# Optimization experiments

Hardware: AMD Instinct MI355X
Metric: run time of the kernel (lower is better)

The kernel has to match this reference:

```python
import jax, jax.numpy as jnp
import numpy as np

N, E, H, IN_FEAT, NUM_GRAPHS, NUM_CLASSES, L, HID = 50000, 600000, 128, 7, 256, 2, 5, 256
EPS_MSG = 1e-7
EPS_SOFTMAX = 1e-16
LN_EPS = 1e-5


def layer_norm(x, g, b):
    mu = jnp.mean(x, axis=-1, keepdims=True)
    var = jnp.mean((x - mu) ** 2, axis=-1, keepdims=True)
    return (x - mu) * jax.lax.rsqrt(var + LN_EPS) * g + b


def setup_inputs() -> dict:
    key = jax.random.key(0)
    ks = jax.random.split(key, 16)
    s = 0.05
    return {
        "x": jax.random.normal(ks[0], (N, IN_FEAT), jnp.float32),
        "edge_index": jax.random.randint(ks[1], (2, E), 0, N),
        "batch": jnp.sort(jax.random.randint(ks[2], (N,), 0, NUM_GRAPHS)),
        "enc_W": jax.random.normal(ks[3], (IN_FEAT, H), jnp.float32) * s,
        "enc_b": jnp.zeros((H,), jnp.float32),
        "t": jnp.ones((L,), jnp.float32),  # learn_t, init t=1.0
        "W1": jax.random.normal(ks[4], (L, H, HID), jnp.float32) * s,
        "b1": jnp.zeros((L, HID), jnp.float32),
        "g1": jnp.ones((L, HID), jnp.float32),
        "bb1": jnp.zeros((L, HID), jnp.float32),
        "W2": jax.random.normal(ks[5], (L, HID, H), jnp.float32) * s,
        "b2": jnp.zeros((L, H), jnp.float32),
        "ln_g": jnp.ones((L, H), jnp.float32),
        "ln_b": jnp.zeros((L, H), jnp.float32),
        "cls_W": jax.random.normal(ks[6], (H, NUM_CLASSES), jnp.float32) * s,
        "cls_b": jnp.zeros((NUM_CLASSES,), jnp.float32),
    }


def reference(x, edge_index, batch, enc_W, enc_b, t, W1, b1, g1, bb1, W2, b2, ln_g, ln_b, cls_W, cls_b):
    n = x.shape[0]
    src, dst = edge_index[0], edge_index[1]  # messages flow src -> dst
    h = x @ enc_W + enc_b  # node_encoder, [N, H]
    for i in range(t.shape[0]):  # DeepGCNLayer, block='res+'
        z = jax.nn.relu(layer_norm(h, ln_g[i], ln_b[i]))
        # GENConv message: relu(x_j) + eps (edge_attr is None)
        msg = jax.nn.relu(z[src]) + EPS_MSG  # [E, H]
        # scatter-softmax aggregation with temperature t
        logits = msg * t[i]
        m = jax.ops.segment_max(logits, dst, num_segments=n)  # [N, H]
        ex = jnp.exp(logits - m[dst])
        den = jax.ops.segment_sum(ex, dst, num_segments=n) + EPS_SOFTMAX
        agg = jax.ops.segment_sum(ex * msg, dst, num_segments=n) / den
        # GENConv update MLP: Linear -> LayerNorm -> ReLU -> Linear on (agg + x)
        out = agg + z
        hm = jax.nn.relu(layer_norm(out @ W1[i] + b1[i], g1[i], bb1[i]))
        h = h + (hm @ W2[i] + b2[i])  # residual
    pooled = jax.ops.segment_sum(h, batch, num_segments=NUM_GRAPHS)  # global_add_pool
    return pooled @ cls_W + cls_b
```

## Files before the change

kernel.cpp:

```cpp
#include <hip/hip_runtime.h>
#include <hip/hip_bf16.h>

#define HD 128
#define HIDD 256
#define EPS_MSG 1e-7f
#define EPS_SM 1e-16f
#define LN_EPS 1e-5f
#define HP2 264
#define LOG2E 1.44269504f

typedef __attribute__((ext_vector_type(8))) short bf16x8;
typedef __attribute__((ext_vector_type(4))) float f32x4;
typedef __attribute__((ext_vector_type(4))) ushort u16x4;

static __device__ __forceinline__ float wave_reduce_sum(float v) {
#pragma unroll
    for (int off = 32; off >= 1; off >>= 1) v += __shfl_xor(v, off, 64);
    return v;
}

static __device__ __forceinline__ float u2f(unsigned v) {
    union { float f; unsigned u; } x;
    x.u = v;
    return x.f;
}
static __device__ __forceinline__ ushort f2bf(float f) {
    __hip_bfloat16 b = __float2bfloat16(f);
    return *(ushort*)&b;
}
static __device__ __forceinline__ unsigned packbf(float lo, float hi) {
    return (unsigned)f2bf(lo) | ((unsigned)f2bf(hi) << 16);
}

__global__ __launch_bounds__(256) void enc_ln_kernel(const float* __restrict__ x,
                                                     const float* __restrict__ W,
                                                     const float* __restrict__ b,
                                                     const float* __restrict__ g,
                                                     const float* __restrict__ bt,
                                                     unsigned* __restrict__ hp,
                                                     unsigned* __restrict__ zp, int N) {
    int node = blockIdx.x * 4 + (threadIdx.x >> 6);
    int lane = threadIdx.x & 63;
    if (node >= N) return;
    float xr[7];
#pragma unroll
    for (int j = 0; j < 7; ++j) xr[j] = x[node * 7 + j];
    float v0 = b[lane], v1 = b[lane + 64];
#pragma unroll
    for (int j = 0; j < 7; ++j) {
        v0 = fmaf(xr[j], W[j * HD + lane], v0);
        v1 = fmaf(xr[j], W[j * HD + lane + 64], v1);
    }
    float s = wave_reduce_sum(v0 + v1);
    float ss = wave_reduce_sum(v0 * v0 + v1 * v1);
    float mu = s * (1.f / 128.f);
    float var = ss * (1.f / 128.f) - mu * mu;
    float rstd = rsqrtf(var + LN_EPS);
    float z0 = fmaxf((v0 - mu) * rstd * g[lane] + bt[lane], 0.f);
    float z1 = fmaxf((v1 - mu) * rstd * g[lane + 64] + bt[lane + 64], 0.f);
    int i0 = (2 * lane) & 63, i1 = (2 * lane + 1) & 63;
    float he_lo = __shfl(v0, i0), ho_lo = __shfl(v0, i1);
    float he_hi = __shfl(v1, i0), ho_hi = __shfl(v1, i1);
    float hce = (lane < 32) ? he_lo : he_hi;
    float hco = (lane < 32) ? ho_lo : ho_hi;
    hp[(size_t)node * 64 + lane] = packbf(hce, hco);
    float e_lo = __shfl(z0, i0), o_lo = __shfl(z0, i1);
    float e_hi = __shfl(z1, i0), o_hi = __shfl(z1, i1);
    float ce = (lane < 32) ? e_lo : e_hi;
    float co = (lane < 32) ? o_lo : o_hi;
    zp[(size_t)node * 64 + lane] = packbf(ce, co);
}

__global__ __launch_bounds__(256) void wconv_kernel(const float* __restrict__ W1,
                                                    const float* __restrict__ W2,
                                                    ushort* __restrict__ W1t,
                                                    ushort* __restrict__ W2t, int L) {
    int gid = blockIdx.x * 256 + threadIdx.x;
    int per = HD * HIDD;
    int tot = L * per;
    if (gid < tot) {
        int l = gid / per, r = gid % per;
        int n = r >> 7, k = r & 127;
        W1t[gid] = f2bf(W1[(size_t)l * per + (size_t)k * HIDD + n]);
    } else if (gid < 2 * tot) {
        int g2 = gid - tot;
        int l = g2 / per, r = g2 % per;
        int n = r >> 8, k = r & 255;
        W2t[g2] = f2bf(W2[(size_t)l * per + (size_t)k * HD + n]);
    }
}

__global__ __launch_bounds__(256) void count_kernel(const int* __restrict__ dst, int* __restrict__ cnt, int E) {
    int e = blockIdx.x * 256 + threadIdx.x;
    if (e < E) atomicAdd(&cnt[dst[e]], 1);
}

__global__ __launch_bounds__(256) void scanA_kernel(const int* __restrict__ cnt, int* __restrict__ row_ptr,
                                                    int* __restrict__ blk_sums, int n) {
    __shared__ int sb[256];
    int tid = threadIdx.x;
    int idx = blockIdx.x * 256 + tid;
    int v = (idx < n) ? cnt[idx] : 0;
    sb[tid] = v;
    __syncthreads();
#pragma unroll
    for (int off = 1; off < 256; off <<= 1) {
        int x = (tid >= off) ? sb[tid - off] : 0;
        __syncthreads();
        sb[tid] += x;
        __syncthreads();
    }
    if (idx < n) row_ptr[idx + 1] = sb[tid];
    if (tid == 255) blk_sums[blockIdx.x] = sb[255];
}

__global__ __launch_bounds__(256) void scanB_kernel(int* __restrict__ blk_sums, int nblk) {
    __shared__ int sb[256];
    int tid = threadIdx.x;
    int v = (tid < nblk) ? blk_sums[tid] : 0;
    sb[tid] = v;
    __syncthreads();
#pragma unroll
    for (int off = 1; off < 256; off <<= 1) {
        int x = (tid >= off) ? sb[tid - off] : 0;
        __syncthreads();
        sb[tid] += x;
        __syncthreads();
    }
    if (tid < nblk) blk_sums[tid] = sb[tid];
}

__global__ __launch_bounds__(256) void scanC_kernel(int* __restrict__ row_ptr, const int* __restrict__ blk_sums,
                                                    int* __restrict__ cursor, int n) {
    int idx = blockIdx.x * 256 + threadIdx.x;
    if (idx == 0) { row_ptr[0] = 0; cursor[0] = 0; }
    if (idx < n) {
        int b = idx >> 8;
        int v = row_ptr[idx + 1] + ((b > 0) ? blk_sums[b - 1] : 0);
        row_ptr[idx + 1] = v;
        if (idx + 1 < n) cursor[idx + 1] = v;
    }
}

__global__ __launch_bounds__(256) void scatter_kernel(const int* __restrict__ src, const int* __restrict__ dst,
                                                      int* __restrict__ cursor, int* __restrict__ esrc, int E) {
    int e = blockIdx.x * 256 + threadIdx.x;
    if (e < E) {
        int v = dst[e];
        int pos = atomicAdd(&cursor[v], 1);
        esrc[pos] = src[e];
    }
}

__global__ __launch_bounds__(256) void agg_kernel(const unsigned* __restrict__ zp,
                                                  const int* __restrict__ row_ptr,
                                                  const int* __restrict__ esrc,
                                                  const float* __restrict__ t_all, int layer,
                                                  unsigned* __restrict__ obuf, int N) {
    int node = __builtin_amdgcn_readfirstlane(blockIdx.x * 4 + (threadIdx.x >> 6));
    int lane = threadIdx.x & 63;
    if (node >= N) return;
    const float tv = t_all[layer];
    const float M = 12.f * fmaxf(tv, 1.f);
    const float tv2 = tv * LOG2E;
    const float mM2 = -M * LOG2E;
    int beg = row_ptr[node], end = row_ptr[node + 1];

    unsigned ps = zp[(size_t)node * 64 + lane];

    float se0 = 0.f, se1 = 0.f, sw0 = 0.f, sw1 = 0.f;
    float te0 = 0.f, te1 = 0.f, tw0 = 0.f, tw1 = 0.f;

#define AGG_EDGE(P, E0, E1, W0, W1)                                   \
    {                                                                  \
        float a0 = u2f((P) << 16) + EPS_MSG;                           \
        float a1 = u2f((P) & 0xffff0000u) + EPS_MSG;                   \
        float x0 = __builtin_amdgcn_exp2f(fmaf(a0, tv2, mM2));         \
        float x1 = __builtin_amdgcn_exp2f(fmaf(a1, tv2, mM2));         \
        E0 += x0;                                                      \
        E1 += x1;                                                      \
        W0 = fmaf(x0, a0, W0);                                         \
        W1 = fmaf(x1, a1, W1);                                         \
    }

    int e = beg;
    unsigned pc0, pc1, pc2, pc3;
    int have = 0;
    if (e + 4 <= end) {
        int s0 = esrc[e], s1 = esrc[e + 1], s2 = esrc[e + 2], s3 = esrc[e + 3];
        pc0 = zp[(size_t)s0 * 64 + lane];
        pc1 = zp[(size_t)s1 * 64 + lane];
        pc2 = zp[(size_t)s2 * 64 + lane];
        pc3 = zp[(size_t)s3 * 64 + lane];
        have = 4;
        e += 4;
    }
    while (have == 4) {
        unsigned pn0, pn1, pn2, pn3;
        int haven = 0;
        if (e + 4 <= end) {
            int s0 = esrc[e], s1 = esrc[e + 1], s2 = esrc[e + 2], s3 = esrc[e + 3];
            pn0 = zp[(size_t)s0 * 64 + lane];
            pn1 = zp[(size_t)s1 * 64 + lane];
            pn2 = zp[(size_t)s2 * 64 + lane];
            pn3 = zp[(size_t)s3 * 64 + lane];
            haven = 4;
            e += 4;
        }
        AGG_EDGE(pc0, se0, se1, sw0, sw1)
        AGG_EDGE(pc1, se0, se1, sw0, sw1)
        AGG_EDGE(pc2, te0, te1, tw0, tw1)
        AGG_EDGE(pc3, te0, te1, tw0, tw1)
        pc0 = pn0; pc1 = pn1; pc2 = pn2; pc3 = pn3;
        have = haven;
    }
    for (; e < end; ++e) {
        unsigned p0 = zp[(size_t)esrc[e] * 64 + lane];
        AGG_EDGE(p0, se0, se1, sw0, sw1)
    }
#undef AGG_EDGE
    se0 += te0; se1 += te1; sw0 += tw0; sw1 += tw1;

    float a0 = (end > beg) ? sw0 / (se0 + EPS_SM) : 0.f;
    float a1 = (end > beg) ? sw1 / (se1 + EPS_SM) : 0.f;
    float z0 = u2f(ps << 16), z1 = u2f(ps & 0xffff0000u);
    obuf[(size_t)node * 64 + lane] = packbf(a0 + z0, a1 + z1);
}

__global__ __launch_bounds__(256) void mlp_kernel(const ushort* __restrict__ obuf,
                                                  unsigned* __restrict__ hp,
                                                  const ushort* __restrict__ W1t, const float* __restrict__ b1,
                                                  const float* __restrict__ g1, const float* __restrict__ bb1,
                                                  const ushort* __restrict__ W2t, const float* __restrict__ b2,
                                                  const float* __restrict__ gnext, const float* __restrict__ btnext,
                                                  unsigned* __restrict__ zp, int fuse,
                                                  int ntiles, int N) {
    __shared__ ushort s_hm[32 * HP2];
    __shared__ float s_part[32 * 8];

    int tid = threadIdx.x;
    int wid = tid >> 6, lane = tid & 63;
    int l15 = lane & 15, q = lane >> 4;

    bf16x8 w1f[4][4];
#pragma unroll
    for (int kk = 0; kk < 4; ++kk)
#pragma unroll
        for (int nb = 0; nb < 4; ++nb)
            w1f[kk][nb] = *(const bf16x8*)&W1t[(size_t)(wid * 64 + nb * 16 + l15) * HD + kk * 32 + q * 8];
    bf16x8 w2f[8][2];
#pragma unroll
    for (int kk = 0; kk < 8; ++kk)
#pragma unroll
        for (int nb = 0; nb < 2; ++nb)
            w2f[kk][nb] = *(const bf16x8*)&W2t[(size_t)(wid * 32 + nb * 16 + l15) * HIDD + kk * 32 + q * 8];

    for (int tile = blockIdx.x; tile < ntiles; tile += gridDim.x) {
        int row0 = tile * 32;

        uint2 hpre[2][2];
        bf16x8 bfr[4][2];
#pragma unroll
        for (int mb = 0; mb < 2; ++mb) {
            int row = row0 + mb * 16 + l15;
            if (row < N) {
#pragma unroll
                for (int nb = 0; nb < 2; ++nb)
                    hpre[mb][nb] = *(const uint2*)&hp[(size_t)row * 64 + wid * 16 + nb * 8 + q * 2];
#pragma unroll
                for (int kk = 0; kk < 4; ++kk)
                    bfr[kk][mb] = *(const bf16x8*)(obuf + (size_t)row * HD + kk * 32 + q * 8);
            } else {
#pragma unroll
                for (int nb = 0; nb < 2; ++nb) { hpre[mb][nb].x = 0u; hpre[mb][nb].y = 0u; }
#pragma unroll
                for (int kk = 0; kk < 4; ++kk) bfr[kk][mb] = (bf16x8)0;
            }
        }
        __syncthreads();

        f32x4 acc1[2][4];
#pragma unroll
        for (int mb = 0; mb < 2; ++mb)
#pragma unroll
            for (int nb = 0; nb < 4; ++nb) acc1[mb][nb] = (f32x4)0.f;
#pragma unroll
        for (int kk = 0; kk < 4; ++kk)
#pragma unroll
            for (int nb = 0; nb < 4; ++nb)
#pragma unroll
                for (int mb = 0; mb < 2; ++mb)
                    acc1[mb][nb] = __builtin_amdgcn_mfma_f32_16x16x32_bf16(w1f[kk][nb], bfr[kk][mb], acc1[mb][nb], 0, 0, 0);

        f32x4 b1v[4];
#pragma unroll
        for (int nb = 0; nb < 4; ++nb) b1v[nb] = *(const f32x4*)&b1[wid * 64 + nb * 16 + q * 4];
#pragma unroll
        for (int mb = 0; mb < 2; ++mb) {
            float s = 0.f, ss = 0.f;
#pragma unroll
            for (int nb = 0; nb < 4; ++nb) {
#pragma unroll
                for (int rg = 0; rg < 4; ++rg) {
                    float v = acc1[mb][nb][rg] + b1v[nb][rg];
                    acc1[mb][nb][rg] = v;
                    s += v;
                    ss += v * v;
                }
            }
            s += __shfl_xor(s, 16, 64);
            s += __shfl_xor(s, 32, 64);
            ss += __shfl_xor(ss, 16, 64);
            ss += __shfl_xor(ss, 32, 64);
            if (q == 0) {
                s_part[(mb * 16 + l15) * 8 + wid * 2] = s;
                s_part[(mb * 16 + l15) * 8 + wid * 2 + 1] = ss;
            }
        }
        __syncthreads();

        f32x4 g1v[4], bbv[4];
#pragma unroll
        for (int nb = 0; nb < 4; ++nb) {
            g1v[nb] = *(const f32x4*)&g1[wid * 64 + nb * 16 + q * 4];
            bbv[nb] = *(const f32x4*)&bb1[wid * 64 + nb * 16 + q * 4];
        }
#pragma unroll
        for (int mb = 0; mb < 2; ++mb) {
            int rl = mb * 16 + l15;
            f32x4 p0 = *(const f32x4*)&s_part[rl * 8];
            f32x4 p1 = *(const f32x4*)&s_part[rl * 8 + 4];
            float S = p0.x + p0.z + p1.x + p1.z;
            float SS = p0.y + p0.w + p1.y + p1.w;
            float mu = S * (1.f / 256.f);
            float var = SS * (1.f / 256.f) - mu * mu;
            float rstd = rsqrtf(var + LN_EPS);
#pragma unroll
            for (int nb = 0; nb < 4; ++nb) {
                u16x4 pk;
#pragma unroll
                for (int rg = 0; rg < 4; ++rg) {
                    float v = fmaxf((acc1[mb][nb][rg] - mu) * rstd * g1v[nb][rg] + bbv[nb][rg], 0.f);
                    pk[rg] = f2bf(v);
                }
                *(u16x4*)&s_hm[rl * HP2 + wid * 64 + nb * 16 + q * 4] = pk;
            }
        }
        __syncthreads();

        f32x4 acc2[2][2];
#pragma unroll
        for (int mb = 0; mb < 2; ++mb)
#pragma unroll
            for (int nb = 0; nb < 2; ++nb) acc2[mb][nb] = (f32x4)0.f;
#pragma unroll
        for (int kk = 0; kk < 8; ++kk) {
            bf16x8 hfr[2];
#pragma unroll
            for (int mb = 0; mb < 2; ++mb)
                hfr[mb] = *(const bf16x8*)&s_hm[(mb * 16 + l15) * HP2 + kk * 32 + q * 8];
#pragma unroll
            for (int nb = 0; nb < 2; ++nb)
#pragma unroll
                for (int mb = 0; mb < 2; ++mb)
                    acc2[mb][nb] = __builtin_amdgcn_mfma_f32_16x16x32_bf16(w2f[kk][nb], hfr[mb], acc2[mb][nb], 0, 0, 0);
        }

        f32x4 b2v[2];
#pragma unroll
        for (int nb = 0; nb < 2; ++nb) b2v[nb] = *(const f32x4*)&b2[wid * 32 + nb * 16 + q * 4];

#pragma unroll
        for (int mb = 0; mb < 2; ++mb) {
            int row = row0 + mb * 16 + l15;
            float s2 = 0.f, ss2 = 0.f;
            if (row < N) {
#pragma unroll
                for (int nb = 0; nb < 2; ++nb) {
                    uint2 hv = hpre[mb][nb];
                    float h0 = u2f(hv.x << 16), h1 = u2f(hv.x & 0xffff0000u);
                    float h2 = u2f(hv.y << 16), h3 = u2f(hv.y & 0xffff0000u);
                    f32x4 v;
                    v[0] = h0 + acc2[mb][nb][0] + b2v[nb][0];
                    v[1] = h1 + acc2[mb][nb][1] + b2v[nb][1];
                    v[2] = h2 + acc2[mb][nb][2] + b2v[nb][2];
                    v[3] = h3 + acc2[mb][nb][3] + b2v[nb][3];
                    s2 += v[0] + v[1] + v[2] + v[3];
                    ss2 += v[0] * v[0] + v[1] * v[1] + v[2] * v[2] + v[3] * v[3];
                    uint2 pk;
                    pk.x = packbf(v[0], v[1]);
                    pk.y = packbf(v[2], v[3]);
                    *(uint2*)&hp[(size_t)row * 64 + wid * 16 + nb * 8 + q * 2] = pk;
                    acc2[mb][nb] = v;
                }
            }
            if (fuse) {
                s2 += __shfl_xor(s2, 16, 64);
                s2 += __shfl_xor(s2, 32, 64);
                ss2 += __shfl_xor(ss2, 16, 64);
                ss2 += __shfl_xor(ss2, 32, 64);
                if (q == 0) {
                    s_part[(mb * 16 + l15) * 8 + wid * 2] = s2;
                    s_part[(mb * 16 + l15) * 8 + wid * 2 + 1] = ss2;
                }
            }
        }

        if (fuse) {
            __syncthreads();
            f32x4 gnv[2], bnv[2];
#pragma unroll
            for (int nb = 0; nb < 2; ++nb) {
                gnv[nb] = *(const f32x4*)&gnext[wid * 32 + nb * 16 + q * 4];
                bnv[nb] = *(const f32x4*)&btnext[wid * 32 + nb * 16 + q * 4];
            }
#pragma unroll
            for (int mb = 0; mb < 2; ++mb) {
                int rl = mb * 16 + l15;
                int row = row0 + rl;
                f32x4 p0 = *(const f32x4*)&s_part[rl * 8];
                f32x4 p1 = *(const f32x4*)&s_part[rl * 8 + 4];
                float S = p0.x + p0.z + p1.x + p1.z;
                float SS = p0.y + p0.w + p1.y + p1.w;
                float mu = S * (1.f / 128.f);
                float var = SS * (1.f / 128.f) - mu * mu;
                float rstd = rsqrtf(var + LN_EPS);
                if (row < N) {
#pragma unroll
                    for (int nb = 0; nb < 2; ++nb) {
                        float z0 = fmaxf((acc2[mb][nb][0] - mu) * rstd * gnv[nb][0] + bnv[nb][0], 0.f);
                        float z1 = fmaxf((acc2[mb][nb][1] - mu) * rstd * gnv[nb][1] + bnv[nb][1], 0.f);
                        float z2 = fmaxf((acc2[mb][nb][2] - mu) * rstd * gnv[nb][2] + bnv[nb][2], 0.f);
                        float z3 = fmaxf((acc2[mb][nb][3] - mu) * rstd * gnv[nb][3] + bnv[nb][3], 0.f);
                        uint2 pk;
                        pk.x = packbf(z0, z1);
                        pk.y = packbf(z2, z3);
                        *(uint2*)&zp[(size_t)row * 64 + wid * 16 + nb * 8 + q * 2] = pk;
                    }
                }
            }
        }
    }
}

__global__ __launch_bounds__(256) void pool_kernel(const unsigned* __restrict__ hp,
                                                   const int* __restrict__ batch, int N,
                                                   float* __restrict__ pooled) {
    __shared__ int sb[2];
    __shared__ float red0[256], red1[256];
    int g = blockIdx.x;
    if (threadIdx.x == 0) {
        int lo = 0, hi = N;
        while (lo < hi) { int mid = (lo + hi) >> 1; if (batch[mid] < g) lo = mid + 1; else hi = mid; }
        sb[0] = lo;
        lo = 0; hi = N;
        int gq = g + 1;
        while (lo < hi) { int mid = (lo + hi) >> 1; if (batch[mid] < gq) lo = mid + 1; else hi = mid; }
        sb[1] = lo;
    }
    __syncthreads();
    int beg = sb[0], end = sb[1];
    int c = threadIdx.x & 63, str = threadIdx.x >> 6;
    float a0 = 0.f, a1 = 0.f;
    for (int r = beg + str; r < end; r += 4) {
        unsigned p = hp[(size_t)r * 64 + c];
        a0 += u2f(p << 16);
        a1 += u2f(p & 0xffff0000u);
    }
    red0[threadIdx.x] = a0;
    red1[threadIdx.x] = a1;
    __syncthreads();
    if (str == 0) {
        float s0 = red0[c] + red0[64 + c] + red0[128 + c] + red0[192 + c];
        float s1 = red1[c] + red1[64 + c] + red1[128 + c] + red1[192 + c];
        pooled[(size_t)g * HD + 2 * c] = s0;
        pooled[(size_t)g * HD + 2 * c + 1] = s1;
    }
}

__global__ __launch_bounds__(256) void cls_kernel(const float* __restrict__ pooled,
                                                  const float* __restrict__ W,
                                                  const float* __restrict__ b,
                                                  float* __restrict__ out, int G) {
    int gid = blockIdx.x * 256 + threadIdx.x;
    if (gid >= G * 2) return;
    int g = gid >> 1, cl = gid & 1;
    float acc = b[cl];
#pragma unroll 8
    for (int k = 0; k < HD; ++k) acc += pooled[g * HD + k] * W[k * 2 + cl];
    out[gid] = acc;
}

extern "C" void kernel_launch(void* const* d_in, const int* in_sizes, int n_in,
                              void* d_out, int out_size, void* d_ws, size_t ws_size,
                              hipStream_t stream) {
    const float* x     = (const float*)d_in[0];
    const int*   eidx  = (const int*)d_in[1];
    const int*   batch = (const int*)d_in[2];
    const float* enc_W = (const float*)d_in[3];
    const float* enc_b = (const float*)d_in[4];
    const float* t_all = (const float*)d_in[5];
    const float* W1    = (const float*)d_in[6];
    const float* b1    = (const float*)d_in[7];
    const float* g1    = (const float*)d_in[8];
    const float* bb1   = (const float*)d_in[9];
    const float* W2    = (const float*)d_in[10];
    const float* b2    = (const float*)d_in[11];
    const float* ln_g  = (const float*)d_in[12];
    const float* ln_b  = (const float*)d_in[13];
    const float* cls_W = (const float*)d_in[14];
    const float* cls_b = (const float*)d_in[15];
    float* out = (float*)d_out;

    const int N = in_sizes[0] / 7;
    const int E = in_sizes[1] / 2;
    const int L = in_sizes[5];
    const int G = out_size / 2;
    const int* src = eidx;
    const int* dst = eidx + E;

    char* p = (char*)d_ws;
    auto alloc = [&](size_t bytes) {
        char* q = p;
        p += (bytes + 255) & ~(size_t)255;
        return q;
    };
    unsigned* hp     = (unsigned*)alloc((size_t)N * 64 * 4);
    unsigned* zp     = (unsigned*)alloc((size_t)N * 64 * 4);
    unsigned* obuf   = (unsigned*)alloc((size_t)N * 64 * 4);
    float*    pooled = (float*)alloc((size_t)G * HD * 4);
    int* cnt      = (int*)alloc((size_t)N * 4);
    int* row_ptr  = (int*)alloc((size_t)(N + 1) * 4);
    int* cursor   = (int*)alloc((size_t)N * 4);
    int* blk_sums = (int*)alloc(256 * 4);
    int* esrc     = (int*)alloc((size_t)E * 4);
    ushort* W1t   = (ushort*)alloc((size_t)L * HD * HIDD * 2);
    ushort* W2t   = (ushort*)alloc((size_t)L * HD * HIDD * 2);

    const int nblkN = (N + 255) / 256;
    const int nblkE = (E + 255) / 256;
    const int ntiles = (N + 31) / 32;

    enc_ln_kernel<<<(N + 3) / 4, 256, 0, stream>>>(x, enc_W, enc_b, ln_g, ln_b, hp, zp, N);
    {
        int tot2 = 2 * L * HD * HIDD;
        wconv_kernel<<<(tot2 + 255) / 256, 256, 0, stream>>>(W1, W2, W1t, W2t, L);
    }

    hipMemsetAsync(cnt, 0, (size_t)N * 4, stream);
    count_kernel<<<nblkE, 256, 0, stream>>>(dst, cnt, E);
    scanA_kernel<<<nblkN, 256, 0, stream>>>(cnt, row_ptr, blk_sums, N);
    scanB_kernel<<<1, 256, 0, stream>>>(blk_sums, nblkN);
    scanC_kernel<<<nblkN, 256, 0, stream>>>(row_ptr, blk_sums, cursor, N);
    scatter_kernel<<<nblkE, 256, 0, stream>>>(src, dst, cursor, esrc, E);

    for (int i = 0; i < L; ++i) {
        agg_kernel<<<(N + 3) / 4, 256, 0, stream>>>(zp, row_ptr, esrc, t_all, i, obuf, N);
        int fuse = (i + 1 < L) ? 1 : 0;
        const float* gn = ln_g + (size_t)(fuse ? i + 1 : i) * HD;
        const float* bn = ln_b + (size_t)(fuse ? i + 1 : i) * HD;
        mlp_kernel<<<512, 256, 0, stream>>>((const ushort*)obuf, hp,
                                            W1t + (size_t)i * HD * HIDD, b1 + (size_t)i * HIDD,
                                            g1 + (size_t)i * HIDD, bb1 + (size_t)i * HIDD,
                                            W2t + (size_t)i * HD * HIDD, b2 + (size_t)i * HD,
                                            gn, bn, zp, fuse, ntiles, N);
    }

    pool_kernel<<<G, 256, 0, stream>>>(hp, batch, N, pooled);
    cls_kernel<<<(G * 2 + 255) / 256, 256, 0, stream>>>(pooled, cls_W, cls_b, out, G);
}
```

Measured before the change: 452.1 us.

## Double-buffer MLP tile loads and stream weights from cache instead of registers

```diff
diff --git a/kernel.cpp b/kernel.cpp
--- a/kernel.cpp
+++ b/kernel.cpp
@@ -238,28 +238,12 @@
     __shared__ ushort s_hm[32 * HP2];
     __shared__ float s_part[32 * 8];
 
-    int tid = threadIdx.x;
-    int wid = tid >> 6, lane = tid & 63;
-    int l15 = lane & 15, q = lane >> 4;
-
-    bf16x8 w1f[4][4];
-#pragma unroll
-    for (int kk = 0; kk < 4; ++kk)
-#pragma unroll
-        for (int nb = 0; nb < 4; ++nb)
-            w1f[kk][nb] = *(const bf16x8*)&W1t[(size_t)(wid * 64 + nb * 16 + l15) * HD + kk * 32 + q * 8];
-    bf16x8 w2f[8][2];
-#pragma unroll
-    for (int kk = 0; kk < 8; ++kk)
-#pragma unroll
-        for (int nb = 0; nb < 2; ++nb)
-            w2f[kk][nb] = *(const bf16x8*)&W2t[(size_t)(wid * 32 + nb * 16 + l15) * HIDD + kk * 32 + q * 8];
-
-    for (int tile = blockIdx.x; tile < ntiles; tile += gridDim.x) {
+    const int tid = threadIdx.x;
+    const int wid = tid >> 6, lane = tid & 63;
+    const int l15 = lane & 15, q = lane >> 4;
+
+    auto loadt = [&](bf16x8 (&bfr)[4][2], uint2 (&hpre)[2][2], int tile) {
         int row0 = tile * 32;
-
-        uint2 hpre[2][2];
-        bf16x8 bfr[4][2];
 #pragma unroll
         for (int mb = 0; mb < 2; ++mb) {
             int row = row0 + mb * 16 + l15;
@@ -277,6 +261,9 @@
                 for (int kk = 0; kk < 4; ++kk) bfr[kk][mb] = (bf16x8)0;
             }
         }
+    };
+
+    auto compute = [&](const bf16x8 (&bfr)[4][2], const uint2 (&hpre)[2][2], int row0) {
         __syncthreads();
 
         f32x4 acc1[2][4];
@@ -285,12 +272,15 @@
 #pragma unroll
             for (int nb = 0; nb < 4; ++nb) acc1[mb][nb] = (f32x4)0.f;
 #pragma unroll
-        for (int kk = 0; kk < 4; ++kk)
-#pragma unroll
-            for (int nb = 0; nb < 4; ++nb)
+        for (int kk = 0; kk < 4; ++kk) {
+#pragma unroll
+            for (int nb = 0; nb < 4; ++nb) {
+                bf16x8 wfr = *(const bf16x8*)&W1t[(size_t)(wid * 64 + nb * 16 + l15) * HD + kk * 32 + q * 8];
 #pragma unroll
                 for (int mb = 0; mb < 2; ++mb)
-                    acc1[mb][nb] = __builtin_amdgcn_mfma_f32_16x16x32_bf16(w1f[kk][nb], bfr[kk][mb], acc1[mb][nb], 0, 0, 0);
+                    acc1[mb][nb] = __builtin_amdgcn_mfma_f32_16x16x32_bf16(wfr, bfr[kk][mb], acc1[mb][nb], 0, 0, 0);
+            }
+        }
 
         f32x4 b1v[4];
 #pragma unroll
@@ -360,16 +350,19 @@
             for (int mb = 0; mb < 2; ++mb)
                 hfr[mb] = *(const bf16x8*)&s_hm[(mb * 16 + l15) * HP2 + kk * 32 + q * 8];
 #pragma unroll
-            for (int nb = 0; nb < 2; ++nb)
+            for (int nb = 0; nb < 2; ++nb) {
+                bf16x8 wfr = *(const bf16x8*)&W2t[(size_t)(wid * 32 + nb * 16 + l15) * HIDD + kk * 32 + q * 8];
 #pragma unroll
                 for (int mb = 0; mb < 2; ++mb)
-                    acc2[mb][nb] = __builtin_amdgcn_mfma_f32_16x16x32_bf16(w2f[kk][nb], hfr[mb], acc2[mb][nb], 0, 0, 0);
+                    acc2[mb][nb] = __builtin_amdgcn_mfma_f32_16x16x32_bf16(wfr, hfr[mb], acc2[mb][nb], 0, 0, 0);
+            }
         }
 
         f32x4 b2v[2];
 #pragma unroll
         for (int nb = 0; nb < 2; ++nb) b2v[nb] = *(const f32x4*)&b2[wid * 32 + nb * 16 + q * 4];
 
+        f32x4 acc2s[2][2];
 #pragma unroll
         for (int mb = 0; mb < 2; ++mb) {
             int row = row0 + mb * 16 + l15;
@@ -391,7 +384,7 @@
                     pk.x = packbf(v[0], v[1]);
                     pk.y = packbf(v[2], v[3]);
                     *(uint2*)&hp[(size_t)row * 64 + wid * 16 + nb * 8 + q * 2] = pk;
-                    acc2[mb][nb] = v;
+                    acc2s[mb][nb] = v;
                 }
             }
             if (fuse) {
@@ -428,10 +421,10 @@
                 if (row < N) {
 #pragma unroll
                     for (int nb = 0; nb < 2; ++nb) {
-                        float z0 = fmaxf((acc2[mb][nb][0] - mu) * rstd * gnv[nb][0] + bnv[nb][0], 0.f);
-                        float z1 = fmaxf((acc2[mb][nb][1] - mu) * rstd * gnv[nb][1] + bnv[nb][1], 0.f);
-                        float z2 = fmaxf((acc2[mb][nb][2] - mu) * rstd * gnv[nb][2] + bnv[nb][2], 0.f);
-                        float z3 = fmaxf((acc2[mb][nb][3] - mu) * rstd * gnv[nb][3] + bnv[nb][3], 0.f);
+                        float z0 = fmaxf((acc2s[mb][nb][0] - mu) * rstd * gnv[nb][0] + bnv[nb][0], 0.f);
+                        float z1 = fmaxf((acc2s[mb][nb][1] - mu) * rstd * gnv[nb][1] + bnv[nb][1], 0.f);
+                        float z2 = fmaxf((acc2s[mb][nb][2] - mu) * rstd * gnv[nb][2] + bnv[nb][2], 0.f);
+                        float z3 = fmaxf((acc2s[mb][nb][3] - mu) * rstd * gnv[nb][3] + bnv[nb][3], 0.f);
                         uint2 pk;
                         pk.x = packbf(z0, z1);
                         pk.y = packbf(z2, z3);
@@ -440,6 +433,26 @@
                 }
             }
         }
+    };
+
+    int t = blockIdx.x;
+    if (t >= ntiles) return;
+
+    bf16x8 bfrA[4][2], bfrB[4][2];
+    uint2 hpreA[2][2], hpreB[2][2];
+
+    loadt(bfrA, hpreA, t);
+    while (true) {
+        int tn = t + gridDim.x;
+        if (tn < ntiles) loadt(bfrB, hpreB, tn);
+        compute(bfrA, hpreA, t * 32);
+        t = tn;
+        if (t >= ntiles) break;
+        tn = t + gridDim.x;
+        if (tn < ntiles) loadt(bfrA, hpreA, tn);
+        compute(bfrB, hpreB, t * 32);
+        t = tn;
+        if (t >= ntiles) break;
     }
 }
 
@@ -559,11 +572,11 @@
         int fuse = (i + 1 < L) ? 1 : 0;
         const float* gn = ln_g + (size_t)(fuse ? i + 1 : i) * HD;
         const float* bn = ln_b + (size_t)(fuse ? i + 1 : i) * HD;
-        mlp_kernel<<<512, 256, 0, stream>>>((const ushort*)obuf, hp,
-                                            W1t + (size_t)i * HD * HIDD, b1 + (size_t)i * HIDD,
-                                            g1 + (size_t)i * HIDD, bb1 + (size_t)i * HIDD,
-                                            W2t + (size_t)i * HD * HIDD, b2 + (size_t)i * HD,
-                                            gn, bn, zp, fuse, ntiles, N);
+        mlp_kernel<<<1024, 256, 0, stream>>>((const ushort*)obuf, hp,
+                                             W1t + (size_t)i * HD * HIDD, b1 + (size_t)i * HIDD,
+                                             g1 + (size_t)i * HIDD, bb1 + (size_t)i * HIDD,
+                                             W2t + (size_t)i * HD * HIDD, b2 + (size_t)i * HD,
+                                             gn, bn, zp, fuse, ntiles, N);
     }
 
     pool_kernel<<<G, 256, 0, stream>>>(hp, batch, N, pooled);
```

New measurement: 545.9 us. 1.21x slower.
